# Optimization experiments

Hardware: AMD Instinct MI355X
Metric: run time of the kernel (lower is better)

Reference implementation:

```python
import jax, jax.numpy as jnp
import numpy as np

B, T, C = 4, 1536, 1536
H, DK, DV = 8, 64, 192
NB = 32  # num_basis per feature class: 192 // (2*3)
MIN_HALF_LIFE = 3.0


def pos_feats_all(distances, seq_len, nb=NB):
    """Enformer positional basis: [exponential, central_mask, gamma], asymmetric.
    distances: int array [L]; returns [L, 6*nb] float32."""
    pos = jnp.abs(distances).astype(jnp.float32)[:, None]  # [L,1]
    sl = jnp.float32(seq_len)
    # exponential
    max_range = jnp.log(sl) / jnp.log(2.0)
    half_life = jnp.power(2.0, jnp.linspace(MIN_HALF_LIFE, max_range, nb))  # [nb]
    f_exp = jnp.exp(-jnp.log(2.0) / half_life * pos)
    # central mask
    widths = jnp.power(2.0, jnp.arange(1, nb + 1, dtype=jnp.float32)) - 1.0
    f_cm = (widths > pos).astype(jnp.float32)
    # gamma
    stddev = sl / (2.0 * nb)
    start_mean = sl / nb
    mean = jnp.linspace(start_mean, sl, nb)
    conc = (mean / stddev) ** 2
    rate = mean / stddev ** 2
    log_unnorm = (conc - 1.0) * jnp.log(pos) - rate * pos  # log(0)=-inf -> exp=0 at pos=0
    log_norm = jax.lax.lgamma(conc) - conc * jnp.log(rate)
    prob = jnp.exp(log_unnorm - log_norm) + 1e-8
    f_gm = prob / jnp.max(prob, axis=0, keepdims=True)
    emb = jnp.concatenate([f_exp, f_cm, f_gm], axis=-1)  # [L, 3*nb]
    sign = jnp.sign(distances).astype(jnp.float32)[:, None]
    return jnp.concatenate([emb, sign * emb], axis=-1)  # [L, 6*nb]


def relative_shift(x):
    """x: [B,H,T,2T-1] -> [B,H,T,T] via the Transformer-XL shift trick."""
    b, h, t, l = x.shape  # l = 2t-1
    x = jnp.pad(x, ((0, 0), (0, 0), (0, 0), (1, 0)))  # [b,h,t,2t]
    x = x.reshape(b, h, l + 1, t)[:, :, 1:, :].reshape(b, h, t, l)
    return x[..., :t]


def setup_inputs() -> dict:
    key = jax.random.key(0)
    ks = jax.random.split(key, 10)
    def dense(k, fi, fo):  # VarianceScaling(scale=2.0)-like init
        return (jax.random.normal(k, (fi, fo), jnp.float32) * np.sqrt(2.0 / fi)).astype(jnp.float32)
    return {
        "x": jax.random.normal(ks[0], (B, T, C), jnp.float32),
        "W_q": dense(ks[1], C, H * DK),
        "W_k": dense(ks[2], C, H * DK),
        "W_v": dense(ks[3], C, H * DV),
        "W_rel_k": dense(ks[4], 6 * NB, H * DK),
        "W_out": dense(ks[5], H * DV, H * DV),
        "b_out": jnp.zeros((H * DV,), jnp.float32),
        "r_w_bias": jax.random.normal(ks[6], (1, H, 1, DK), jnp.float32) * np.sqrt(2.0 / DK),
        "r_r_bias": jax.random.normal(ks[7], (1, H, 1, DK), jnp.float32) * np.sqrt(2.0 / DK),
    }


def reference(x, W_q, W_k, W_v, W_rel_k, W_out, b_out, r_w_bias, r_r_bias):
    b, t, _ = x.shape
    def heads(w, d):  # [b,t,H*d] -> [b,H,t,d]
        return (x @ w).reshape(b, t, H, d).transpose(0, 2, 1, 3)
    Q = heads(W_q, DK) * (DK ** -0.5)  # scaling applied before biases
    K = heads(W_k, DK)
    V = heads(W_v, DV)
    distances = jnp.arange(-t + 1, t)  # [2t-1]
    pe = pos_feats_all(distances, t)  # [2t-1, 6*NB]
    rK = (pe @ W_rel_k).reshape(2 * t - 1, H, DK).transpose(1, 0, 2)  # [H, 2t-1, DK]
    content = jnp.einsum('bhqd,bhkd->bhqk', Q + r_w_bias, K)
    rel = jnp.einsum('bhqd,hld->bhql', Q + r_r_bias, rK)  # [b,H,t,2t-1]
    logits = content + relative_shift(rel)
    attn = jax.nn.softmax(logits, axis=-1)
    out = jnp.einsum('bhqk,bhkd->bhqd', attn, V)  # [b,H,t,DV]
    out = out.transpose(0, 2, 1, 3).reshape(b, t, H * DV)
    return out @ W_out + b_out
```

## Files before the change

### kernel.cpp

```cpp
#include <hip/hip_runtime.h>
#include <hip/hip_bf16.h>
#include <math.h>

#define BB 4
#define TT 1536
#define CC 1536
#define HH 8
#define DKk 64
#define DVv 192
#define NBASIS 32
#define LREL 3071
#define MROWS 6144

typedef short short8 __attribute__((ext_vector_type(8)));
typedef float floatx4 __attribute__((ext_vector_type(4)));

static __device__ inline short f2bf(float f) {
  __hip_bfloat16 h = __float2bfloat16(f);
  return *reinterpret_cast<short*>(&h);
}

static __device__ inline void gload_lds16(const __hip_bfloat16* g, __hip_bfloat16* l) {
  __builtin_amdgcn_global_load_lds(
      (const __attribute__((address_space(1))) unsigned int*)g,
      (__attribute__((address_space(3))) unsigned int*)l, 16, 0, 0);
}

__global__ void detect_kernel(const void* __restrict__ x, int* __restrict__ flag) {
  if (threadIdx.x == 0 && blockIdx.x == 0) {
    const __hip_bfloat16* h = (const __hip_bfloat16*)x;
    int cnt = 0;
    for (int i = 0; i < 64; ++i) {
      float v = fabsf((float)h[2 * i]);
      if (v > 1e-5f && v < 256.0f) cnt++;
    }
    *flag = (cnt >= 32) ? 1 : 0;
  }
}

__global__ __launch_bounds__(256) void convert_kernel(const void* __restrict__ src,
                                                      float* __restrict__ dst, int n,
                                                      const int* __restrict__ flag) {
  const int i = blockIdx.x * 256 + threadIdx.x;
  if (i >= n) return;
  if (*flag) dst[i] = (float)((const __hip_bfloat16*)src)[i];
  else       dst[i] = ((const float*)src)[i];
}

__global__ __launch_bounds__(256) void convbf_kernel(const void* __restrict__ src,
                                                     __hip_bfloat16* __restrict__ dst, int n,
                                                     const int* __restrict__ flag) {
  const int i = blockIdx.x * 256 + threadIdx.x;
  if (i >= n) return;
  if (*flag) dst[i] = ((const __hip_bfloat16*)src)[i];
  else       dst[i] = __float2bfloat16(((const float*)src)[i]);
}

__global__ __launch_bounds__(256) void wt_kernel(const void* __restrict__ src,
                                                 __hip_bfloat16* __restrict__ dst,
                                                 int K, int N, const int* __restrict__ flag) {
  __shared__ __hip_bfloat16 tile[64][68];
  const int tid = threadIdx.x;
  const int k0 = blockIdx.y * 64, n0 = blockIdx.x * 64;
  const bool bf = (*flag != 0);
  {
    const int r = tid >> 2, c0 = (tid & 3) * 16;
    if (bf) {
      const __hip_bfloat16* sp = (const __hip_bfloat16*)src + (size_t)(k0 + r) * N + n0 + c0;
#pragma unroll
      for (int u = 0; u < 16; ++u) tile[r][c0 + u] = sp[u];
    } else {
      const float* sp = (const float*)src + (size_t)(k0 + r) * N + n0 + c0;
#pragma unroll
      for (int u = 0; u < 16; ++u) tile[r][c0 + u] = __float2bfloat16(sp[u]);
    }
  }
  __syncthreads();
  {
    const int nr = tid >> 2, c0 = (tid & 3) * 16;
    __hip_bfloat16* dp = dst + (size_t)(n0 + nr) * K + k0 + c0;
#pragma unroll
    for (int u = 0; u < 16; ++u) dp[u] = tile[c0 + u][nr];
  }
}

__global__ void gmax_kernel(double* __restrict__ gmax) {
  const int j = blockIdx.x;
  const double mean = 48.0 + 1488.0 * (double)j / 31.0;
  const double conc = (mean / 24.0) * (mean / 24.0);
  const double rate = mean / 576.0;
  const double log_norm = lgamma(conc) - conc * log(rate);
  double mx = 1e-8;
  for (int pos = 1 + threadIdx.x; pos <= 1535; pos += 256) {
    double p = exp((conc - 1.0) * log((double)pos) - rate * (double)pos - log_norm) + 1e-8;
    mx = fmax(mx, p);
  }
  __shared__ double red[256];
  red[threadIdx.x] = mx;
  __syncthreads();
  for (int s = 128; s > 0; s >>= 1) {
    if (threadIdx.x < s) red[threadIdx.x] = fmax(red[threadIdx.x], red[threadIdx.x + s]);
    __syncthreads();
  }
  if (threadIdx.x == 0) gmax[j] = red[0];
}

__global__ void pe_kernel(float* __restrict__ pe, const double* __restrict__ gmax) {
  const int l = blockIdx.x;
  const int f = threadIdx.x;
  const int dist = l - (TT - 1);
  const int pos = dist < 0 ? -dist : dist;
  const int base = f % 96;
  const int cls = base / 32;
  const int j = base % 32;
  double v;
  if (cls == 0) {
    const double max_range = log(1536.0) / log(2.0);
    const double e = 3.0 + (max_range - 3.0) * (double)j / 31.0;
    const double hl = exp2(e);
    v = exp2(-(double)pos / hl);
  } else if (cls == 1) {
    const double width = exp2((double)(j + 1)) - 1.0;
    v = (width > (double)pos) ? 1.0 : 0.0;
  } else {
    const double mean = 48.0 + 1488.0 * (double)j / 31.0;
    const double conc = (mean / 24.0) * (mean / 24.0);
    const double rate = mean / 576.0;
    double p;
    if (pos == 0) {
      p = 1e-8;
    } else {
      const double log_norm = lgamma(conc) - conc * log(rate);
      p = exp((conc - 1.0) * log((double)pos) - rate * (double)pos - log_norm) + 1e-8;
    }
    v = p / gmax[j];
  }
  float out = (float)v;
  if (f >= 96) {
    float sgn = (dist > 0) ? 1.f : (dist < 0 ? -1.f : 0.f);
    out *= sgn;
  }
  pe[(size_t)l * 192 + f] = out;
}

__global__ __launch_bounds__(512) void relk_kernel(const float* __restrict__ pe,
                                                   const float* __restrict__ Wrk,
                                                   __hip_bfloat16* __restrict__ rKl) {
  __shared__ float pes[8][192];
  const int l0 = blockIdx.x * 8;
  const int nrows = (LREL - l0) < 8 ? (LREL - l0) : 8;
  const int tid = threadIdx.x;
  for (int idx = tid; idx < nrows * 192; idx += 512) {
    int r = idx / 192, f = idx % 192;
    pes[r][f] = pe[(size_t)(l0 + r) * 192 + f];
  }
  __syncthreads();
  float acc[8] = {0.f, 0.f, 0.f, 0.f, 0.f, 0.f, 0.f, 0.f};
  for (int f = 0; f < 192; ++f) {
    float w = Wrk[(size_t)f * 512 + tid];
#pragma unroll
    for (int r = 0; r < 8; ++r) acc[r] += pes[r][f] * w;
  }
  const int h = tid >> 6, d = tid & 63;
  for (int r = 0; r < nrows; ++r)
    rKl[((size_t)h * LREL + (l0 + r)) * 64 + d] = __float2bfloat16(acc[r]);
}

template <int MODE, bool BIAS>
__global__ __launch_bounds__(256) void gemm_mfma(const __hip_bfloat16* __restrict__ A,
                                                 const __hip_bfloat16* __restrict__ Bt,
                                                 void* __restrict__ Cout,
                                                 void* __restrict__ Cout2,
                                                 void* __restrict__ Cout3,
                                                 const float* __restrict__ bias,
                                                 int M, int N, int K,
                                                 const int* __restrict__ flag) {
  __shared__ __align__(16) __hip_bfloat16 As[128 * 64];
  __shared__ __align__(16) __hip_bfloat16 Bs[128 * 64];
  const int tid = threadIdx.x;
  const int w = tid >> 6, lane = tid & 63;
  const int quad = lane >> 4, l16 = lane & 15;
  const int wm = w >> 1, wn = w & 1;
  const int row0 = blockIdx.y * 128, col0 = blockIdx.x * 128;

  const floatx4 vzero = {0.f, 0.f, 0.f, 0.f};
  floatx4 acc[4][4];
#pragma unroll
  for (int i = 0; i < 4; ++i)
#pragma unroll
    for (int j = 0; j < 4; ++j) acc[i][j] = vzero;

  const int sr = lane >> 3;
  const int sg = (lane & 7) ^ sr;
  const __hip_bfloat16* ag = A + (size_t)(row0 + w * 32 + sr) * K + sg * 8;
  const __hip_bfloat16* bg = Bt + (size_t)(col0 + w * 32 + sr) * K + sg * 8;
  __hip_bfloat16* as_ = As + w * 32 * 64;
  __hip_bfloat16* bs_ = Bs + w * 32 * 64;

  for (int k0 = 0; k0 < K; k0 += 64) {
    __syncthreads();
#pragma unroll
    for (int i = 0; i < 4; ++i) {
      gload_lds16(ag + (size_t)(i * 8) * K + k0, as_ + i * 8 * 64);
      gload_lds16(bg + (size_t)(i * 8) * K + k0, bs_ + i * 8 * 64);
    }
    __syncthreads();
#pragma unroll
    for (int ks = 0; ks < 2; ++ks) {
      const int xr = (((ks * 4 + quad) ^ (l16 & 7)) << 3);
      short8 aF[4], bF[4];
#pragma unroll
      for (int mt = 0; mt < 4; ++mt)
        aF[mt] = *(const short8*)(As + (wm * 64 + mt * 16 + l16) * 64 + xr);
#pragma unroll
      for (int nt = 0; nt < 4; ++nt)
        bF[nt] = *(const short8*)(Bs + (wn * 64 + nt * 16 + l16) * 64 + xr);
#pragma unroll
      for (int mt = 0; mt < 4; ++mt)
#pragma unroll
        for (int nt = 0; nt < 4; ++nt)
          acc[mt][nt] = __builtin_amdgcn_mfma_f32_16x16x32_bf16(aF[mt], bF[nt], acc[mt][nt], 0, 0, 0);
    }
  }

  const bool obf = (MODE == 2) ? (*flag != 0) : false;
#pragma unroll
  for (int mt = 0; mt < 4; ++mt) {
#pragma unroll
    for (int r = 0; r < 4; ++r) {
      const int row = row0 + wm * 64 + mt * 16 + quad * 4 + r;
#pragma unroll
      for (int nt = 0; nt < 4; ++nt) {
        const int col = col0 + wn * 64 + nt * 16 + l16;
        float v = acc[mt][nt][r];
        if (BIAS) v += bias[col];
        if (MODE == 0) {
          ((float*)Cout)[(size_t)row * N + col] = v;
        } else if (MODE == 1) {
          ((__hip_bfloat16*)Cout)[(size_t)row * N + col] = __float2bfloat16(v);
        } else if (MODE == 2) {
          if (obf) ((__hip_bfloat16*)Cout)[(size_t)row * N + col] = __float2bfloat16(v);
          else     ((float*)Cout)[(size_t)row * N + col] = v;
        } else {
          if (col < 512)
            ((float*)Cout)[(size_t)row * 512 + col] = v;
          else if (col < 1024)
            ((__hip_bfloat16*)Cout2)[(size_t)row * 512 + (col - 512)] = __float2bfloat16(v);
          else
            ((__hip_bfloat16*)Cout3)[(size_t)row * 1536 + (col - 1024)] = __float2bfloat16(v);
        }
      }
    }
  }
}

__global__ __launch_bounds__(256) void kfrag_kernel(const __hip_bfloat16* __restrict__ Kbf,
                                                    __hip_bfloat16* __restrict__ Kfrag) {
  const int widx = blockIdx.x * 256 + threadIdx.x;
  const int lane = widx & 63;
  const int ks = (widx >> 6) & 1;
  const int kt = (widx >> 7) % 96;
  const int bh = (widx >> 7) / 96;
  const int b = bh >> 3, h = bh & 7;
  const __hip_bfloat16* src = Kbf + ((size_t)(b * TT + kt * 16 + (lane & 15))) * 512
                              + h * 64 + ks * 32 + (lane >> 4) * 8;
  *(uint4*)(Kfrag + (size_t)widx * 8) = *(const uint4*)src;
}

__global__ __launch_bounds__(256) void rkfrag_kernel(const __hip_bfloat16* __restrict__ rKl,
                                                     __hip_bfloat16* __restrict__ rKfrag) {
  const int widx = blockIdx.x * 256 + threadIdx.x;
  const int lane = widx & 63;
  const int ks = (widx >> 6) & 1;
  const int lt = (widx >> 7) % 192;
  const int h = (widx >> 7) / 192;
  int l = lt * 16 + (lane & 15);
  if (l > 3070) l = 3070;
  const __hip_bfloat16* src = rKl + ((size_t)h * LREL + l) * 64 + ks * 32 + (lane >> 4) * 8;
  *(uint4*)(rKfrag + (size_t)widx * 8) = *(const uint4*)src;
}

__global__ __launch_bounds__(256) void vfrag_kernel(const __hip_bfloat16* __restrict__ Vbf,
                                                    __hip_bfloat16* __restrict__ Vfrag) {
  int bid = blockIdx.x;
  int vt3 = bid % 3; int kb = (bid / 3) % 24; int h = (bid / 72) & 7; int b = bid / 576;
  const int bh = b * 8 + h;
  __shared__ __hip_bfloat16 tile[64][72];
  const int tid = threadIdx.x;
  {
    int r = tid >> 2, c0 = (tid & 3) * 16;
    const __hip_bfloat16* src = Vbf + (size_t)(b * TT + kb * 64 + r) * 1536 + h * 192 + vt3 * 64 + c0;
#pragma unroll
    for (int u = 0; u < 16; ++u) tile[r][c0 + u] = src[u];
  }
  __syncthreads();
#pragma unroll
  for (int u = 0; u < 2; ++u) {
    const int w512 = u * 256 + tid;
    const int vtl = w512 >> 7;
    const int ks = (w512 >> 6) & 1;
    const int ln = w512 & 63;
    const int qd = ln >> 4, s16 = ln & 15;
    union { uint4 u4; unsigned short us[8]; } pk;
#pragma unroll
    for (int j = 0; j < 8; ++j)
      pk.us[j] = *(const unsigned short*)&tile[ks * 32 + qd * 8 + j][vtl * 16 + s16];
    __hip_bfloat16* dst = Vfrag +
        (((size_t)(bh * 24 + kb) * 12 + vt3 * 4 + vtl) * 2 + ks) * 512 + (size_t)ln * 8;
    *(uint4*)dst = pk.u4;
  }
}

__global__ __launch_bounds__(256, 3) void attn_frag(
    const float* __restrict__ tmpQ,
    const float* __restrict__ rwb,
    const float* __restrict__ rrb,
    const __hip_bfloat16* __restrict__ Kfrag,
    const __hip_bfloat16* __restrict__ rKfrag,
    const __hip_bfloat16* __restrict__ Vfrag,
    __hip_bfloat16* __restrict__ O)
{
  const int tid = threadIdx.x;
  const int w = tid >> 6, lane = tid & 63;
  const int quad = lane >> 4, l16 = lane & 15;
  const int le8 = lane * 8;
  const int o = (blockIdx.x & 7) * 96 + (blockIdx.x >> 3);
  const int qt = o % 24;
  const int h = (o / 24) & 7;
  const int b = o / 192;
  const int bh = b * 8 + h;
  const int q0 = qt * 64;

  __shared__ __align__(16) char sm[49152];
  __hip_bfloat16* Klds  = (__hip_bfloat16*)sm;
  __hip_bfloat16* rKlds = (__hip_bfloat16*)(sm + 8192);
  __hip_bfloat16* Vlds  = (__hip_bfloat16*)(sm + 24576);
  __hip_bfloat16* Rbuf  = (__hip_bfloat16*)sm;
  __hip_bfloat16* Ptile = (__hip_bfloat16*)(sm + 10752);
  float* alphaS = (float*)(sm + 19968);
  float* lrowS  = (float*)(sm + 20224);

  short8 aQw[2], aQr[2];
  {
    const int qrow = q0 + w * 16 + l16;
    const float* qp = tmpQ + (size_t)(b * TT + qrow) * 512 + h * 64;
#pragma unroll
    for (int ks = 0; ks < 2; ++ks) {
#pragma unroll
      for (int j = 0; j < 8; ++j) {
        const int d = ks * 32 + quad * 8 + j;
        const float qv = qp[d] * 0.125f;
        aQw[ks][j] = f2bf(qv + rwb[h * 64 + d]);
        aQr[ks][j] = f2bf(qv + rrb[h * 64 + d]);
      }
    }
  }

  const floatx4 vzero = {0.f, 0.f, 0.f, 0.f};
  floatx4 Oacc[12];
#pragma unroll
  for (int i = 0; i < 12; ++i) Oacc[i] = vzero;
  float mrow[4], lrow[4];
#pragma unroll
  for (int r = 0; r < 4; ++r) { mrow[r] = -INFINITY; lrow[r] = 0.f; }

  const __hip_bfloat16* kSrc = Kfrag + (size_t)bh * 98304 + le8;
  const __hip_bfloat16* rSrc = rKfrag + (size_t)h * 196608
                               + (size_t)((1472 - q0) >> 4) * 1024 + le8;
  const __hip_bfloat16* vSrc = Vfrag + (size_t)bh * 294912 + le8;

  const int jt0 = 3 - w;

  for (int k0 = 0; k0 < TT; k0 += 64) {
    __syncthreads();
    {
      const __hip_bfloat16* kIt = kSrc + (size_t)(k0 >> 4) * 1024;
      const __hip_bfloat16* rIt = rSrc + (size_t)(k0 >> 4) * 1024;
      const __hip_bfloat16* vIt = vSrc + (size_t)(k0 >> 6) * 12288;
      if (w == 0) {
#pragma unroll
        for (int i = 0; i < 8; ++i) gload_lds16(kIt + i * 512, Klds + i * 512);
#pragma unroll
        for (int i = 0; i < 4; ++i) gload_lds16(rIt + i * 512, rKlds + i * 512);
      } else if (w == 1) {
#pragma unroll
        for (int i = 4; i < 16; ++i) gload_lds16(rIt + i * 512, rKlds + i * 512);
      } else if (w == 2) {
#pragma unroll
        for (int i = 0; i < 12; ++i) gload_lds16(vIt + i * 512, Vlds + i * 512);
      } else {
#pragma unroll
        for (int i = 12; i < 24; ++i) gload_lds16(vIt + i * 512, Vlds + i * 512);
      }
    }
    __syncthreads();

    floatx4 S[4], R[5];
#pragma unroll
    for (int i = 0; i < 4; ++i) S[i] = vzero;
#pragma unroll
    for (int i = 0; i < 5; ++i) R[i] = vzero;

    __builtin_amdgcn_s_setprio(1);
#pragma unroll
    for (int kt = 0; kt < 4; ++kt) {
#pragma unroll
      for (int ks = 0; ks < 2; ++ks) {
        short8 bK = *(const short8*)(Klds + (kt * 2 + ks) * 512 + le8);
        S[kt] = __builtin_amdgcn_mfma_f32_16x16x32_bf16(aQw[ks], bK, S[kt], 0, 0, 0);
      }
    }
#pragma unroll
    for (int i = 0; i < 5; ++i) {
      const int jt = jt0 + i;
#pragma unroll
      for (int ks = 0; ks < 2; ++ks) {
        short8 bR = *(const short8*)(rKlds + (jt * 2 + ks) * 512 + le8);
        R[i] = __builtin_amdgcn_mfma_f32_16x16x32_bf16(aQr[ks], bR, R[i], 0, 0, 0);
      }
    }
    __builtin_amdgcn_s_setprio(0);
    __syncthreads();

#pragma unroll
    for (int i = 0; i < 5; ++i) {
#pragma unroll
      for (int r = 0; r < 4; ++r) {
        const int row = w * 16 + quad * 4 + r;
        Rbuf[row * 84 + i * 16 + l16] = __float2bfloat16(R[i][r]);
      }
    }
#pragma unroll
    for (int kt = 0; kt < 4; ++kt) {
#pragma unroll
      for (int r = 0; r < 4; ++r) {
        const int row = w * 16 + quad * 4 + r;
        const int cj = kt * 16 + l16 + 15 - quad * 4 - r;
        S[kt][r] += (float)Rbuf[row * 84 + cj];
      }
    }

    float alpha[4];
#pragma unroll
    for (int r = 0; r < 4; ++r) {
      float mx = fmaxf(fmaxf(S[0][r], S[1][r]), fmaxf(S[2][r], S[3][r]));
#pragma unroll
      for (int off = 8; off > 0; off >>= 1) mx = fmaxf(mx, __shfl_xor(mx, off));
      const float nm = fmaxf(mrow[r], mx);
      alpha[r] = __expf(mrow[r] - nm);
      mrow[r] = nm;
      float ps = 0.f;
#pragma unroll
      for (int kt = 0; kt < 4; ++kt) {
        const float p = __expf(S[kt][r] - nm);
        S[kt][r] = p;
        ps += p;
      }
#pragma unroll
      for (int off = 8; off > 0; off >>= 1) ps += __shfl_xor(ps, off);
      lrow[r] = lrow[r] * alpha[r] + ps;
    }
#pragma unroll
    for (int kt = 0; kt < 4; ++kt) {
#pragma unroll
      for (int r = 0; r < 4; ++r) {
        const int row = w * 16 + quad * 4 + r;
        Ptile[row * 72 + kt * 16 + l16] = __float2bfloat16(S[kt][r]);
      }
    }
    if (l16 == 0) {
#pragma unroll
      for (int r = 0; r < 4; ++r) alphaS[w * 16 + quad * 4 + r] = alpha[r];
    }
    __syncthreads();

#pragma unroll
    for (int qf = 0; qf < 4; ++qf) {
      const floatx4 al = *(const floatx4*)(alphaS + qf * 16 + quad * 4);
#pragma unroll
      for (int vtl = 0; vtl < 3; ++vtl)
#pragma unroll
        for (int r = 0; r < 4; ++r) Oacc[qf * 3 + vtl][r] *= al[r];
    }

    short8 aP[4][2];
#pragma unroll
    for (int qf = 0; qf < 4; ++qf)
#pragma unroll
      for (int ks = 0; ks < 2; ++ks)
        aP[qf][ks] = *(const short8*)(Ptile + (qf * 16 + l16) * 72 + ks * 32 + quad * 8);

    __builtin_amdgcn_s_setprio(1);
#pragma unroll
    for (int vtl = 0; vtl < 3; ++vtl) {
#pragma unroll
      for (int ks = 0; ks < 2; ++ks) {
        short8 bV = *(const short8*)(Vlds + ((w * 3 + vtl) * 2 + ks) * 512 + le8);
#pragma unroll
        for (int qf = 0; qf < 4; ++qf)
          Oacc[qf * 3 + vtl] = __builtin_amdgcn_mfma_f32_16x16x32_bf16(aP[qf][ks], bV, Oacc[qf * 3 + vtl], 0, 0, 0);
      }
    }
    __builtin_amdgcn_s_setprio(0);
  }

  if (l16 == 0) {
#pragma unroll
    for (int r = 0; r < 4; ++r) lrowS[w * 16 + quad * 4 + r] = lrow[r];
  }
  __syncthreads();
#pragma unroll
  for (int qf = 0; qf < 4; ++qf) {
    const floatx4 lv = *(const floatx4*)(lrowS + qf * 16 + quad * 4);
#pragma unroll
    for (int r = 0; r < 4; ++r) {
      const float inv = 1.f / lv[r];
      const int qrow = q0 + qf * 16 + quad * 4 + r;
      __hip_bfloat16* op = O + (size_t)(b * TT + qrow) * 1536 + h * 192 + w * 48;
#pragma unroll
      for (int vtl = 0; vtl < 3; ++vtl)
        op[vtl * 16 + l16] = __float2bfloat16(Oacc[qf * 3 + vtl][r] * inv);
    }
  }
}

extern "C" void kernel_launch(void* const* d_in, const int* in_sizes, int n_in,
                              void* d_out, int out_size, void* d_ws, size_t ws_size,
                              hipStream_t stream) {
  const void* x     = d_in[0];
  const void* W_q   = d_in[1];
  const void* W_k   = d_in[2];
  const void* W_v   = d_in[3];
  const void* W_rel = d_in[4];
  const void* W_out = d_in[5];
  const void* b_out = d_in[6];
  const void* r_w_b = d_in[7];
  const void* r_r_b = d_in[8];

  float* ws = (float*)d_ws;
  int*    flag = (int*)d_ws;
  double* gmax = (double*)(ws + 16);
  float* pe    = ws + 16 + 64;
  float* WrelF = pe    + (size_t)LREL * 192;
  float* boutF = WrelF + (size_t)192 * 512;
  float* rwbF  = boutF + 1536;
  float* rrbF  = rwbF + 512;
  float* tmpQ  = rrbF + 512;
  __hip_bfloat16* xBf  = (__hip_bfloat16*)(tmpQ + (size_t)MROWS * 512);
  __hip_bfloat16* WqT  = xBf  + (size_t)MROWS * 1536;
  __hip_bfloat16* WkT  = WqT  + (size_t)512 * 1536;
  __hip_bfloat16* WvT  = WkT  + (size_t)512 * 1536;
  __hip_bfloat16* WoT  = WvT  + (size_t)1536 * 1536;
  __hip_bfloat16* Kbf  = WoT  + (size_t)1536 * 1536;
  __hip_bfloat16* Vbf  = Kbf  + (size_t)MROWS * 512;
  __hip_bfloat16* Vfrag= Vbf  + (size_t)MROWS * 1536;
  __hip_bfloat16* Obf  = Vfrag + (size_t)32 * 192 * 1536;
  __hip_bfloat16* rKl  = Obf  + (size_t)MROWS * 1536;
  char* endp = (char*)(rKl + (size_t)HH * LREL * 64);
  if (ws_size < (size_t)(endp - (char*)d_ws)) return;

  __hip_bfloat16* Kfrag  = xBf;
  __hip_bfloat16* rKfrag = xBf + (size_t)3145728;

  detect_kernel<<<1, 64, 0, stream>>>(x, flag);

  auto conv = [&](const void* src, float* dst, int n) {
    convert_kernel<<<(n + 255) / 256, 256, 0, stream>>>(src, dst, n, flag);
  };
  conv(W_rel, WrelF, 192 * 512);
  conv(b_out, boutF, 1536);
  conv(r_w_b, rwbF,  512);
  conv(r_r_b, rrbF,  512);

  convbf_kernel<<<(MROWS * 1536 + 255) / 256, 256, 0, stream>>>(x, xBf, MROWS * 1536, flag);

  wt_kernel<<<dim3(512 / 64, 1536 / 64), 256, 0, stream>>>(W_q, WqT, 1536, 512, flag);
  wt_kernel<<<dim3(512 / 64, 1536 / 64), 256, 0, stream>>>(W_k, WkT, 1536, 512, flag);
  wt_kernel<<<dim3(1536 / 64, 1536 / 64), 256, 0, stream>>>(W_v, WvT, 1536, 1536, flag);
  wt_kernel<<<dim3(1536 / 64, 1536 / 64), 256, 0, stream>>>(W_out, WoT, 1536, 1536, flag);

  gmax_kernel<<<32, 256, 0, stream>>>(gmax);
  pe_kernel<<<LREL, 192, 0, stream>>>(pe, gmax);
  relk_kernel<<<(LREL + 7) / 8, 512, 0, stream>>>(pe, WrelF, rKl);

  gemm_mfma<3, false><<<dim3(2560 / 128, MROWS / 128), 256, 0, stream>>>(
      xBf, WqT, tmpQ, Kbf, Vbf, nullptr, MROWS, 2560, CC, flag);

  kfrag_kernel<<<1536, 256, 0, stream>>>(Kbf, Kfrag);
  rkfrag_kernel<<<768, 256, 0, stream>>>(rKl, rKfrag);
  vfrag_kernel<<<2304, 256, 0, stream>>>(Vbf, Vfrag);

  attn_frag<<<768, 256, 0, stream>>>(tmpQ, rwbF, rrbF, Kfrag, rKfrag, Vfrag, Obf);

  gemm_mfma<2, true><<<dim3(1536 / 128, MROWS / 128), 256, 0, stream>>>(
      Obf, WoT, d_out, nullptr, nullptr, boutF, MROWS, 1536, CC, flag);
}
```

Before: 461.1 us.

## Load V fragments directly into registers and remap GEMM block order

```diff
diff --git a/kernel.cpp b/kernel.cpp
--- a/kernel.cpp
+++ b/kernel.cpp
@@ -181,7 +181,11 @@
   const int w = tid >> 6, lane = tid & 63;
   const int quad = lane >> 4, l16 = lane & 15;
   const int wm = w >> 1, wn = w & 1;
-  const int row0 = blockIdx.y * 128, col0 = blockIdx.x * 128;
+  const int gx = gridDim.x;
+  const int nwg = gx * gridDim.y;
+  const int id = blockIdx.y * gx + blockIdx.x;
+  const int o = (id & 7) * (nwg >> 3) + (id >> 3);
+  const int row0 = (o / gx) * 128, col0 = (o % gx) * 128;
 
   const floatx4 vzero = {0.f, 0.f, 0.f, 0.f};
   floatx4 acc[4][4];
@@ -331,14 +335,13 @@
   const int bh = b * 8 + h;
   const int q0 = qt * 64;
 
-  __shared__ __align__(16) char sm[49152];
+  __shared__ __align__(16) char sm[45056];
   __hip_bfloat16* Klds  = (__hip_bfloat16*)sm;
   __hip_bfloat16* rKlds = (__hip_bfloat16*)(sm + 8192);
-  __hip_bfloat16* Vlds  = (__hip_bfloat16*)(sm + 24576);
-  __hip_bfloat16* Rbuf  = (__hip_bfloat16*)sm;
-  __hip_bfloat16* Ptile = (__hip_bfloat16*)(sm + 10752);
-  float* alphaS = (float*)(sm + 19968);
-  float* lrowS  = (float*)(sm + 20224);
+  __hip_bfloat16* Rbuf  = (__hip_bfloat16*)(sm + 24576);
+  __hip_bfloat16* Ptile = (__hip_bfloat16*)(sm + 35328);
+  float* alphaS = (float*)(sm + 44544);
+  float* lrowS  = (float*)(sm + 44800);
 
   short8 aQw[2], aQr[2];
   {
@@ -367,33 +370,42 @@
   const __hip_bfloat16* kSrc = Kfrag + (size_t)bh * 98304 + le8;
   const __hip_bfloat16* rSrc = rKfrag + (size_t)h * 196608
                                + (size_t)((1472 - q0) >> 4) * 1024 + le8;
-  const __hip_bfloat16* vSrc = Vfrag + (size_t)bh * 294912 + le8;
+  const __hip_bfloat16* vSrc = Vfrag + (size_t)bh * 294912;
 
   const int jt0 = 3 - w;
 
-  for (int k0 = 0; k0 < TT; k0 += 64) {
+  for (int t = 0; t < 24; ++t) {
     __syncthreads();
     {
-      const __hip_bfloat16* kIt = kSrc + (size_t)(k0 >> 4) * 1024;
-      const __hip_bfloat16* rIt = rSrc + (size_t)(k0 >> 4) * 1024;
-      const __hip_bfloat16* vIt = vSrc + (size_t)(k0 >> 6) * 12288;
+      const __hip_bfloat16* kIt = kSrc + (size_t)(t * 4) * 1024;
+      const __hip_bfloat16* rIt = rSrc + (size_t)(t * 4) * 1024;
       if (w == 0) {
 #pragma unroll
-        for (int i = 0; i < 8; ++i) gload_lds16(kIt + i * 512, Klds + i * 512);
+        for (int i = 0; i < 6; ++i) gload_lds16(kIt + i * 512, Klds + i * 512);
+      } else if (w == 1) {
+#pragma unroll
+        for (int i = 6; i < 8; ++i) gload_lds16(kIt + i * 512, Klds + i * 512);
 #pragma unroll
         for (int i = 0; i < 4; ++i) gload_lds16(rIt + i * 512, rKlds + i * 512);
-      } else if (w == 1) {
-#pragma unroll
-        for (int i = 4; i < 16; ++i) gload_lds16(rIt + i * 512, rKlds + i * 512);
       } else if (w == 2) {
 #pragma unroll
-        for (int i = 0; i < 12; ++i) gload_lds16(vIt + i * 512, Vlds + i * 512);
+        for (int i = 4; i < 10; ++i) gload_lds16(rIt + i * 512, rKlds + i * 512);
       } else {
 #pragma unroll
-        for (int i = 12; i < 24; ++i) gload_lds16(vIt + i * 512, Vlds + i * 512);
+        for (int i = 10; i < 16; ++i) gload_lds16(rIt + i * 512, rKlds + i * 512);
       }
     }
     __syncthreads();
+
+    short8 vReg[3][2];
+    {
+      const __hip_bfloat16* vIt = vSrc + (size_t)t * 12288;
+#pragma unroll
+      for (int vtl = 0; vtl < 3; ++vtl)
+#pragma unroll
+        for (int ks = 0; ks < 2; ++ks)
+          vReg[vtl][ks] = *(const short8*)(vIt + ((w * 3 + vtl) * 2 + ks) * 512 + le8);
+    }
 
     floatx4 S[4], R[5];
 #pragma unroll
@@ -495,10 +507,9 @@
     for (int vtl = 0; vtl < 3; ++vtl) {
 #pragma unroll
       for (int ks = 0; ks < 2; ++ks) {
-        short8 bV = *(const short8*)(Vlds + ((w * 3 + vtl) * 2 + ks) * 512 + le8);
 #pragma unroll
         for (int qf = 0; qf < 4; ++qf)
-          Oacc[qf * 3 + vtl] = __builtin_amdgcn_mfma_f32_16x16x32_bf16(aP[qf][ks], bV, Oacc[qf * 3 + vtl], 0, 0, 0);
+          Oacc[qf * 3 + vtl] = __builtin_amdgcn_mfma_f32_16x16x32_bf16(aP[qf][ks], vReg[vtl][ks], Oacc[qf * 3 + vtl], 0, 0, 0);
       }
     }
     __builtin_amdgcn_s_setprio(0);
```

Result: faster. 434.2 us (-5.8%).
